# Kernel tuning notes

Measured on AMD Instinct MI355X. Metric: run time of the kernel, lower is better.

Reference implementation:

```python
import jax, jax.numpy as jnp
import numpy as np

N, E = 50000, 800000
IN, HID, OUT, T = 96, 128, 64, 8
THETA = 0.5


def setup_inputs() -> dict:
    key = jax.random.key(0)
    ks = jax.random.split(key, 8)
    x = jax.random.normal(ks[0], (N, IN), dtype=jnp.float32)
    edge_weight = jax.random.uniform(ks[1], (E,), dtype=jnp.float32)
    W1 = jax.random.normal(ks[2], (IN, HID), dtype=jnp.float32) * (2.0 / np.sqrt(IN + HID))
    W2 = jax.random.normal(ks[3], (HID, OUT), dtype=jnp.float32) * (2.0 / np.sqrt(HID + OUT))
    # Bernoulli(1 - theta) masks, fixed per MC sample (created in __init__)
    mask1 = (jax.random.uniform(ks[4], (T, IN, HID)) < (1.0 - THETA)).astype(jnp.float32)
    mask2 = (jax.random.uniform(ks[5], (T, HID, OUT)) < (1.0 - THETA)).astype(jnp.float32)
    src = jax.random.randint(ks[6], (E,), 0, N, dtype=jnp.int32)
    dst = jax.random.randint(ks[7], (E,), 0, N, dtype=jnp.int32)
    return {"x": x, "edge_weight": edge_weight, "W1": W1, "W2": W2,
            "mask1": mask1, "mask2": mask2, "src": src, "dst": dst}


def _spmm(feat, edge_weight, src, dst, n_nodes):
    # u_mul_e('feat','edge_weight') followed by fn.sum onto dst nodes
    msg = feat[src] * edge_weight[:, None]          # [E, D]
    return jax.ops.segment_sum(msg, dst, num_segments=n_nodes)  # [N, D]


def reference(x, edge_weight, W1, W2, mask1, mask2, src, dst):
    n = x.shape[0]
    # first aggregation is mask-independent -> compute once, share across T samples
    agg1 = _spmm(x, edge_weight, src, dst, n)       # [N, IN]

    def per_sample(m1, m2):
        h = jax.nn.relu(agg1 @ (W1 * m1))           # [N, HID]
        agg2 = _spmm(h, edge_weight, src, dst, n)   # [N, HID]
        return agg2 @ (W2 * m2)                     # [N, OUT]

    # stack of the T per-sample outputs (torch version returns a list)
    return jax.vmap(per_sample)(mask1, mask2)       # [T, N, OUT]
```

## Files before the change

### kernel.cpp

```cpp
#include <hip/hip_runtime.h>

#define N_NODES 50000
#define N_EDGES 800000
#define IN_F 96
#define HID_F 128
#define OUT_F 64
#define T_S 8
#define SCAN_B 196

typedef __attribute__((ext_vector_type(8))) short short8;
typedef __attribute__((ext_vector_type(4))) float float4v;

__device__ __forceinline__ float bf2f(unsigned short h) {
    unsigned u = ((unsigned)h) << 16;
    float f;
    __builtin_memcpy(&f, &u, 4);
    return f;
}
__device__ __forceinline__ unsigned short f2bf(float f) {
    unsigned u;
    __builtin_memcpy(&u, &f, 4);
    unsigned r = (u + 0x7fffu + ((u >> 16) & 1u)) >> 16;
    return (unsigned short)r;
}
__device__ __forceinline__ float bf_lo(unsigned u) {
    unsigned v = u << 16;
    float f;
    __builtin_memcpy(&f, &v, 4);
    return f;
}
__device__ __forceinline__ float bf_hi(unsigned u) {
    unsigned v = u & 0xffff0000u;
    float f;
    __builtin_memcpy(&f, &v, 4);
    return f;
}

__global__ void k_count(const int* __restrict__ dst, int* __restrict__ cnt) {
    int e = blockIdx.x * 256 + threadIdx.x;
    if (e < N_EDGES) atomicAdd(&cnt[dst[e]], 1);
}

__global__ __launch_bounds__(256) void k_scan1(const int* __restrict__ cnt,
                                               int* __restrict__ excl,
                                               int* __restrict__ blockSums) {
    __shared__ int buf[256];
    int tid = threadIdx.x;
    int idx = blockIdx.x * 256 + tid;
    int v = (idx < N_NODES) ? cnt[idx] : 0;
    buf[tid] = v;
    __syncthreads();
    for (int off = 1; off < 256; off <<= 1) {
        int t = buf[tid];
        int u = (tid >= off) ? buf[tid - off] : 0;
        __syncthreads();
        buf[tid] = t + u;
        __syncthreads();
    }
    int incl = buf[tid];
    if (idx < N_NODES) excl[idx] = incl - v;
    if (tid == 255) blockSums[blockIdx.x] = incl;
}

__global__ __launch_bounds__(256) void k_scan2(const int* __restrict__ blockSums,
                                               int* __restrict__ blockOff) {
    __shared__ int buf[256];
    int tid = threadIdx.x;
    int v = (tid < SCAN_B) ? blockSums[tid] : 0;
    buf[tid] = v;
    __syncthreads();
    for (int off = 1; off < 256; off <<= 1) {
        int t = buf[tid];
        int u = (tid >= off) ? buf[tid - off] : 0;
        __syncthreads();
        buf[tid] = t + u;
        __syncthreads();
    }
    if (tid < SCAN_B) blockOff[tid] = buf[tid] - v;
}

__global__ __launch_bounds__(256) void k_scan3(const int* __restrict__ excl,
                                               const int* __restrict__ blockOff,
                                               int* __restrict__ row_ptr,
                                               int* __restrict__ cursor) {
    int idx = blockIdx.x * 256 + threadIdx.x;
    if (idx < N_NODES) {
        int p = excl[idx] + blockOff[blockIdx.x];
        row_ptr[idx] = p;
        cursor[idx] = p;
    }
    if (idx == 0) row_ptr[N_NODES] = N_EDGES;
}

__global__ void k_fill(const int* __restrict__ src, const int* __restrict__ dst,
                       const float* __restrict__ ew, int* __restrict__ cursor,
                       int* __restrict__ csr_src, float* __restrict__ csr_w) {
    int e = blockIdx.x * 256 + threadIdx.x;
    if (e < N_EDGES) {
        int d = dst[e];
        int pos = atomicAdd(&cursor[d], 1);
        csr_src[pos] = src[e];
        csr_w[pos] = ew[e];
    }
}

__global__ void k_xb(const float* __restrict__ x, unsigned short* __restrict__ xb) {
    int i = blockIdx.x * 256 + threadIdx.x;
    int idx = i * 4;
    if (idx < N_NODES * IN_F) {
        float4 v = *(const float4*)(x + idx);
        uint2 r;
        r.x = (unsigned)f2bf(v.x) | ((unsigned)f2bf(v.y) << 16);
        r.y = (unsigned)f2bf(v.z) | ((unsigned)f2bf(v.w) << 16);
        *(uint2*)(xb + idx) = r;
    }
}

__global__ __launch_bounds__(256) void k_spmm1(const unsigned short* __restrict__ xb,
                                               const int* __restrict__ row_ptr,
                                               const int* __restrict__ csr_src,
                                               const float* __restrict__ csr_w,
                                               unsigned short* __restrict__ agg1) {
    int wave = threadIdx.x >> 6, lane = threadIdx.x & 63;
    int node = blockIdx.x * 4 + wave;
    if (lane >= 48) return;
    int beg = row_ptr[node], end = row_ptr[node + 1];
    const unsigned* xrow = (const unsigned*)xb;
    float a0 = 0.f, a1 = 0.f;
    int e = beg;
    for (; e + 7 < end; e += 8) {
        int s[8];
        float wv[8];
        unsigned d[8];
#pragma unroll
        for (int i = 0; i < 8; i++) {
            s[i] = csr_src[e + i];
            wv[i] = csr_w[e + i];
        }
#pragma unroll
        for (int i = 0; i < 8; i++) d[i] = xrow[(size_t)s[i] * 48 + lane];
#pragma unroll
        for (int i = 0; i < 8; i++) {
            a0 = fmaf(wv[i], bf_lo(d[i]), a0);
            a1 = fmaf(wv[i], bf_hi(d[i]), a1);
        }
    }
    for (; e < end; e++) {
        int s = csr_src[e];
        float wv = csr_w[e];
        unsigned d = xrow[(size_t)s * 48 + lane];
        a0 = fmaf(wv, bf_lo(d), a0);
        a1 = fmaf(wv, bf_hi(d), a1);
    }
    ((unsigned*)agg1)[(size_t)node * 48 + lane] =
        (unsigned)f2bf(a0) | ((unsigned)f2bf(a1) << 16);
}

__global__ void k_wprep(const float* __restrict__ W1, const float* __restrict__ W2,
                        const float* __restrict__ m1, const float* __restrict__ m2,
                        unsigned short* __restrict__ wf) {
    int gid = blockIdx.x * 256 + threadIdx.x;
    if (gid >= T_S * 20480) return;
    int t = gid / 20480;
    int idx = gid % 20480;
    float val;
    if (idx < 12288) {
        int j = idx & 7, lane = (idx >> 3) & 63, fr = idx >> 9;
        int kk = fr >> 3, nt = fr & 7;
        int k = kk * 32 + (lane >> 4) * 8 + j;
        int n = nt * 16 + (lane & 15);
        val = W1[k * HID_F + n] * m1[((size_t)t * IN_F + k) * HID_F + n];
    } else {
        int i2 = idx - 12288;
        int j = i2 & 7, lane = (i2 >> 3) & 63, fr = i2 >> 9;
        int kk = fr >> 2, ot = fr & 3;
        int k = kk * 32 + (lane >> 4) * 8 + j;
        int o = ot * 16 + (lane & 15);
        val = W2[k * OUT_F + o] * m2[((size_t)t * HID_F + k) * OUT_F + o];
    }
    wf[gid] = f2bf(val);
}

__global__ __launch_bounds__(256) void k_gemm(const unsigned short* __restrict__ agg1,
                                              const unsigned short* __restrict__ wfrags,
                                              unsigned short* __restrict__ P, int tBase,
                                              int nodeStride, int tMul) {
    __shared__ __align__(16) unsigned short ldsW[20480];
    __shared__ __align__(16) unsigned short ldsH[4][2176];
    int t = tBase + blockIdx.y;
    const uint4* wsrc = (const uint4*)(wfrags + (size_t)t * 20480);
    uint4* wdst = (uint4*)ldsW;
    for (int i = threadIdx.x; i < 2560; i += 256) wdst[i] = wsrc[i];
    __syncthreads();

    int wave = threadIdx.x >> 6, lane = threadIdx.x & 63;
    int quad = lane >> 4, l15 = lane & 15;
    int node = blockIdx.x * 64 + wave * 16 + l15;
    bool v = node < N_NODES;

    short8 a[3];
    if (v) {
        const unsigned short* ap = agg1 + (size_t)node * IN_F;
        a[0] = *(const short8*)(ap + 0 * 32 + quad * 8);
        a[1] = *(const short8*)(ap + 1 * 32 + quad * 8);
        a[2] = *(const short8*)(ap + 2 * 32 + quad * 8);
    } else {
        short8 z = {0, 0, 0, 0, 0, 0, 0, 0};
        a[0] = z; a[1] = z; a[2] = z;
    }

    for (int nt = 0; nt < 8; nt++) {
        float4v acc = {0.f, 0.f, 0.f, 0.f};
        for (int kk = 0; kk < 3; kk++) {
            short8 w = *(const short8*)&ldsW[(kk * 8 + nt) * 512 + lane * 8];
            acc = __builtin_amdgcn_mfma_f32_16x16x32_bf16(w, a[kk], acc, 0, 0, 0);
        }
        unsigned h0 = f2bf(fmaxf(acc[0], 0.f));
        unsigned h1 = f2bf(fmaxf(acc[1], 0.f));
        unsigned h2 = f2bf(fmaxf(acc[2], 0.f));
        unsigned h3 = f2bf(fmaxf(acc[3], 0.f));
        uint2 pk;
        pk.x = h0 | (h1 << 16);
        pk.y = h2 | (h3 << 16);
        *(uint2*)&ldsH[wave][l15 * 136 + nt * 16 + quad * 4] = pk;
    }

    short8 hf[4];
    for (int kk = 0; kk < 4; kk++)
        hf[kk] = *(const short8*)&ldsH[wave][l15 * 136 + kk * 32 + quad * 8];

    unsigned short* Pt = P + (size_t)node * nodeStride + (size_t)t * tMul;
    for (int ot = 0; ot < 4; ot++) {
        float4v acc = {0.f, 0.f, 0.f, 0.f};
        for (int kk = 0; kk < 4; kk++) {
            short8 w = *(const short8*)&ldsW[12288 + (kk * 4 + ot) * 512 + lane * 8];
            acc = __builtin_amdgcn_mfma_f32_16x16x32_bf16(w, hf[kk], acc, 0, 0, 0);
        }
        if (v) {
            uint2 pk;
            pk.x = (unsigned)f2bf(acc[0]) | ((unsigned)f2bf(acc[1]) << 16);
            pk.y = (unsigned)f2bf(acc[2]) | ((unsigned)f2bf(acc[3]) << 16);
            *(uint2*)(Pt + ot * 16 + quad * 4) = pk;
        }
    }
}

__global__ __launch_bounds__(256) void k_spmm2(const unsigned short* __restrict__ P,
                                               const int* __restrict__ row_ptr,
                                               const int* __restrict__ csr_src,
                                               const float* __restrict__ csr_w,
                                               float* __restrict__ out) {
    int wave = threadIdx.x >> 6, lane = threadIdx.x & 63;
    int node = blockIdx.x * 4 + wave;
    int beg = row_ptr[node], end = row_ptr[node + 1];
    const uint4* Pl = (const uint4*)P + lane;
    float acc[8] = {0.f, 0.f, 0.f, 0.f, 0.f, 0.f, 0.f, 0.f};
    int e = beg;
    for (; e + 7 < end; e += 8) {
        int s[8];
        float wv[8];
        uint4 d[8];
#pragma unroll
        for (int i = 0; i < 8; i++) {
            s[i] = csr_src[e + i];
            wv[i] = csr_w[e + i];
        }
#pragma unroll
        for (int i = 0; i < 8; i++) d[i] = Pl[(size_t)s[i] * 64];
#pragma unroll
        for (int i = 0; i < 8; i++) {
            acc[0] = fmaf(wv[i], bf_lo(d[i].x), acc[0]);
            acc[1] = fmaf(wv[i], bf_hi(d[i].x), acc[1]);
            acc[2] = fmaf(wv[i], bf_lo(d[i].y), acc[2]);
            acc[3] = fmaf(wv[i], bf_hi(d[i].y), acc[3]);
            acc[4] = fmaf(wv[i], bf_lo(d[i].z), acc[4]);
            acc[5] = fmaf(wv[i], bf_hi(d[i].z), acc[5]);
            acc[6] = fmaf(wv[i], bf_lo(d[i].w), acc[6]);
            acc[7] = fmaf(wv[i], bf_hi(d[i].w), acc[7]);
        }
    }
    for (; e < end; e++) {
        int s = csr_src[e];
        float wv = csr_w[e];
        uint4 d = Pl[(size_t)s * 64];
        acc[0] = fmaf(wv, bf_lo(d.x), acc[0]);
        acc[1] = fmaf(wv, bf_hi(d.x), acc[1]);
        acc[2] = fmaf(wv, bf_lo(d.y), acc[2]);
        acc[3] = fmaf(wv, bf_hi(d.y), acc[3]);
        acc[4] = fmaf(wv, bf_lo(d.z), acc[4]);
        acc[5] = fmaf(wv, bf_hi(d.z), acc[5]);
        acc[6] = fmaf(wv, bf_lo(d.w), acc[6]);
        acc[7] = fmaf(wv, bf_hi(d.w), acc[7]);
    }
    int t = lane >> 3, o = (lane & 7) * 8;
    float* op = out + ((size_t)t * N_NODES + node) * OUT_F + o;
    float4 v0 = {acc[0], acc[1], acc[2], acc[3]};
    float4 v1 = {acc[4], acc[5], acc[6], acc[7]};
    *(float4*)op = v0;
    *(float4*)(op + 4) = v1;
}

__global__ __launch_bounds__(512) void k_spmm2_1t(const unsigned short* __restrict__ P,
                                                  const int* __restrict__ row_ptr,
                                                  const int* __restrict__ csr_src,
                                                  const float* __restrict__ csr_w,
                                                  float* __restrict__ out) {
    int node = blockIdx.x * 8 + (threadIdx.x >> 6);
    int o = threadIdx.x & 63;
    if (node >= N_NODES) return;
    int beg = row_ptr[node], end = row_ptr[node + 1];
    const unsigned short* Pt = P + o;
    float a0 = 0.f, a1 = 0.f, a2 = 0.f, a3 = 0.f;
    int e = beg;
    for (; e + 3 < end; e += 4) {
        int s0 = csr_src[e], s1 = csr_src[e + 1], s2 = csr_src[e + 2], s3 = csr_src[e + 3];
        float w0 = csr_w[e], w1 = csr_w[e + 1], w2 = csr_w[e + 2], w3 = csr_w[e + 3];
        a0 += w0 * bf2f(Pt[(size_t)s0 * OUT_F]);
        a1 += w1 * bf2f(Pt[(size_t)s1 * OUT_F]);
        a2 += w2 * bf2f(Pt[(size_t)s2 * OUT_F]);
        a3 += w3 * bf2f(Pt[(size_t)s3 * OUT_F]);
    }
    for (; e < end; e++) a0 += csr_w[e] * bf2f(Pt[(size_t)csr_src[e] * OUT_F]);
    out[(size_t)node * OUT_F + o] = a0 + a1 + a2 + a3;
}

extern "C" void kernel_launch(void* const* d_in, const int* in_sizes, int n_in,
                              void* d_out, int out_size, void* d_ws, size_t ws_size,
                              hipStream_t stream) {
    const float* x = (const float*)d_in[0];
    const float* ew = (const float*)d_in[1];
    const float* W1 = (const float*)d_in[2];
    const float* W2 = (const float*)d_in[3];
    const float* m1 = (const float*)d_in[4];
    const float* m2 = (const float*)d_in[5];
    const int* src = (const int*)d_in[6];
    const int* dst = (const int*)d_in[7];
    float* out = (float*)d_out;

    char* w = (char*)d_ws;
    size_t off = 0;
    auto alloc = [&](size_t bytes) -> void* {
        void* p = (void*)(w + off);
        off += (bytes + 255) & ~(size_t)255;
        return p;
    };
    int* cnt = (int*)alloc((size_t)N_NODES * 4);
    int* row_ptr = (int*)alloc((size_t)(N_NODES + 1) * 4);
    int* cursor = (int*)alloc((size_t)N_NODES * 4);
    int* excl = (int*)alloc((size_t)N_NODES * 4);
    int* blockSums = (int*)alloc((size_t)SCAN_B * 4);
    int* blockOff = (int*)alloc((size_t)SCAN_B * 4);
    int* csr_src = (int*)alloc((size_t)N_EDGES * 4);
    float* csr_w = (float*)alloc((size_t)N_EDGES * 4);
    unsigned short* agg1 = (unsigned short*)alloc((size_t)N_NODES * IN_F * 2);
    unsigned short* wf = (unsigned short*)alloc((size_t)T_S * 20480 * 2);

    size_t unionBase = off;
    size_t pBytesBatched = (size_t)T_S * N_NODES * OUT_F * 2;
    size_t xbBytes = (size_t)N_NODES * IN_F * 2;
    bool batched = ws_size >= unionBase + (pBytesBatched > xbBytes ? pBytesBatched : xbBytes);
    unsigned short* xb = (unsigned short*)(w + unionBase);
    unsigned short* P = (unsigned short*)(w + unionBase);
    if (!batched) {
        xb = (unsigned short*)(w + unionBase);
        P = (unsigned short*)(w + unionBase + ((xbBytes + 255) & ~(size_t)255));
    }

    hipMemsetAsync(cnt, 0, (size_t)N_NODES * 4, stream);
    k_count<<<N_EDGES / 256, 256, 0, stream>>>(dst, cnt);
    k_scan1<<<SCAN_B, 256, 0, stream>>>(cnt, excl, blockSums);
    k_scan2<<<1, 256, 0, stream>>>(blockSums, blockOff);
    k_scan3<<<SCAN_B, 256, 0, stream>>>(excl, blockOff, row_ptr, cursor);
    k_fill<<<N_EDGES / 256, 256, 0, stream>>>(src, dst, ew, cursor, csr_src, csr_w);
    k_xb<<<(N_NODES * IN_F / 4 + 255) / 256, 256, 0, stream>>>(x, xb);
    k_spmm1<<<N_NODES / 4, 256, 0, stream>>>(xb, row_ptr, csr_src, csr_w, agg1);
    k_wprep<<<(T_S * 20480) / 256, 256, 0, stream>>>(W1, W2, m1, m2, wf);

    if (batched) {
        k_gemm<<<dim3(782, 8), 256, 0, stream>>>(agg1, wf, P, 0, T_S * OUT_F, OUT_F);
        k_spmm2<<<N_NODES / 4, 256, 0, stream>>>(P, row_ptr, csr_src, csr_w, out);
    } else {
        for (int t = 0; t < T_S; t++) {
            k_gemm<<<dim3(782, 1), 256, 0, stream>>>(agg1, wf, P, t, OUT_F, 0);
            k_spmm2_1t<<<6250, 512, 0, stream>>>(P, row_ptr, csr_src, csr_w,
                                                 out + (size_t)t * N_NODES * OUT_F);
        }
    }
}
```

Baseline: 427.7 us.

## Interleave CSR src/weight, add nontemporal hints, amortize GEMM weight load over 4 tiles

Packs csr_src and csr_w into one 8-byte array so each edge needs a single load, and marks the streaming loads and stores nontemporal to keep the gather data resident in cache. The GEMM kernel now handles four 64-node tiles per block, so the 40KB weight copy into LDS happens a quarter as often. A 4-wide remainder loop is added to the SpMM kernels. The trade-off is fewer blocks in the GEMM grid, which lowers parallelism, and nontemporal hints may help or hurt depending on how the cache handles them.

```diff
diff --git a/kernel.cpp b/kernel.cpp
--- a/kernel.cpp
+++ b/kernel.cpp
@@ -10,6 +10,8 @@
 
 typedef __attribute__((ext_vector_type(8))) short short8;
 typedef __attribute__((ext_vector_type(4))) float float4v;
+typedef __attribute__((ext_vector_type(2))) unsigned uint2v;
+typedef __attribute__((ext_vector_type(4))) unsigned uint4v;
 
 __device__ __forceinline__ float bf2f(unsigned short h) {
     unsigned u = ((unsigned)h) << 16;
@@ -94,13 +96,15 @@
 
 __global__ void k_fill(const int* __restrict__ src, const int* __restrict__ dst,
                        const float* __restrict__ ew, int* __restrict__ cursor,
-                       int* __restrict__ csr_src, float* __restrict__ csr_w) {
+                       uint2v* __restrict__ csr) {
     int e = blockIdx.x * 256 + threadIdx.x;
     if (e < N_EDGES) {
         int d = dst[e];
         int pos = atomicAdd(&cursor[d], 1);
-        csr_src[pos] = src[e];
-        csr_w[pos] = ew[e];
+        uint2v c;
+        c.x = (unsigned)src[e];
+        c.y = __float_as_uint(ew[e]);
+        __builtin_nontemporal_store(c, &csr[pos]);
     }
 }
 
@@ -108,18 +112,17 @@
     int i = blockIdx.x * 256 + threadIdx.x;
     int idx = i * 4;
     if (idx < N_NODES * IN_F) {
-        float4 v = *(const float4*)(x + idx);
-        uint2 r;
+        float4v v = __builtin_nontemporal_load((const float4v*)(x + idx));
+        uint2v r;
         r.x = (unsigned)f2bf(v.x) | ((unsigned)f2bf(v.y) << 16);
         r.y = (unsigned)f2bf(v.z) | ((unsigned)f2bf(v.w) << 16);
-        *(uint2*)(xb + idx) = r;
+        *(uint2v*)(xb + idx) = r;
     }
 }
 
 __global__ __launch_bounds__(256) void k_spmm1(const unsigned short* __restrict__ xb,
                                                const int* __restrict__ row_ptr,
-                                               const int* __restrict__ csr_src,
-                                               const float* __restrict__ csr_w,
+                                               const uint2v* __restrict__ csr,
                                                unsigned short* __restrict__ agg1) {
     int wave = threadIdx.x >> 6, lane = threadIdx.x & 63;
     int node = blockIdx.x * 4 + wave;
@@ -129,31 +132,42 @@
     float a0 = 0.f, a1 = 0.f;
     int e = beg;
     for (; e + 7 < end; e += 8) {
-        int s[8];
-        float wv[8];
+        uint2v c[8];
         unsigned d[8];
 #pragma unroll
+        for (int i = 0; i < 8; i++) c[i] = __builtin_nontemporal_load(&csr[e + i]);
+#pragma unroll
+        for (int i = 0; i < 8; i++) d[i] = xrow[(size_t)c[i].x * 48 + lane];
+#pragma unroll
         for (int i = 0; i < 8; i++) {
-            s[i] = csr_src[e + i];
-            wv[i] = csr_w[e + i];
-        }
-#pragma unroll
-        for (int i = 0; i < 8; i++) d[i] = xrow[(size_t)s[i] * 48 + lane];
-#pragma unroll
-        for (int i = 0; i < 8; i++) {
-            a0 = fmaf(wv[i], bf_lo(d[i]), a0);
-            a1 = fmaf(wv[i], bf_hi(d[i]), a1);
+            float wv = __uint_as_float(c[i].y);
+            a0 = fmaf(wv, bf_lo(d[i]), a0);
+            a1 = fmaf(wv, bf_hi(d[i]), a1);
+        }
+    }
+    for (; e + 3 < end; e += 4) {
+        uint2v c[4];
+        unsigned d[4];
+#pragma unroll
+        for (int i = 0; i < 4; i++) c[i] = __builtin_nontemporal_load(&csr[e + i]);
+#pragma unroll
+        for (int i = 0; i < 4; i++) d[i] = xrow[(size_t)c[i].x * 48 + lane];
+#pragma unroll
+        for (int i = 0; i < 4; i++) {
+            float wv = __uint_as_float(c[i].y);
+            a0 = fmaf(wv, bf_lo(d[i]), a0);
+            a1 = fmaf(wv, bf_hi(d[i]), a1);
         }
     }
     for (; e < end; e++) {
-        int s = csr_src[e];
-        float wv = csr_w[e];
-        unsigned d = xrow[(size_t)s * 48 + lane];
+        uint2v c = __builtin_nontemporal_load(&csr[e]);
+        float wv = __uint_as_float(c.y);
+        unsigned d = xrow[(size_t)c.x * 48 + lane];
         a0 = fmaf(wv, bf_lo(d), a0);
         a1 = fmaf(wv, bf_hi(d), a1);
     }
-    ((unsigned*)agg1)[(size_t)node * 48 + lane] =
-        (unsigned)f2bf(a0) | ((unsigned)f2bf(a1) << 16);
+    unsigned pk = (unsigned)f2bf(a0) | ((unsigned)f2bf(a1) << 16);
+    __builtin_nontemporal_store(pk, (unsigned*)agg1 + (size_t)node * 48 + lane);
 }
 
 __global__ void k_wprep(const float* __restrict__ W1, const float* __restrict__ W2,
@@ -195,94 +209,113 @@
 
     int wave = threadIdx.x >> 6, lane = threadIdx.x & 63;
     int quad = lane >> 4, l15 = lane & 15;
-    int node = blockIdx.x * 64 + wave * 16 + l15;
-    bool v = node < N_NODES;
-
-    short8 a[3];
-    if (v) {
-        const unsigned short* ap = agg1 + (size_t)node * IN_F;
-        a[0] = *(const short8*)(ap + 0 * 32 + quad * 8);
-        a[1] = *(const short8*)(ap + 1 * 32 + quad * 8);
-        a[2] = *(const short8*)(ap + 2 * 32 + quad * 8);
-    } else {
-        short8 z = {0, 0, 0, 0, 0, 0, 0, 0};
-        a[0] = z; a[1] = z; a[2] = z;
-    }
-
-    for (int nt = 0; nt < 8; nt++) {
-        float4v acc = {0.f, 0.f, 0.f, 0.f};
-        for (int kk = 0; kk < 3; kk++) {
-            short8 w = *(const short8*)&ldsW[(kk * 8 + nt) * 512 + lane * 8];
-            acc = __builtin_amdgcn_mfma_f32_16x16x32_bf16(w, a[kk], acc, 0, 0, 0);
-        }
-        unsigned h0 = f2bf(fmaxf(acc[0], 0.f));
-        unsigned h1 = f2bf(fmaxf(acc[1], 0.f));
-        unsigned h2 = f2bf(fmaxf(acc[2], 0.f));
-        unsigned h3 = f2bf(fmaxf(acc[3], 0.f));
-        uint2 pk;
-        pk.x = h0 | (h1 << 16);
-        pk.y = h2 | (h3 << 16);
-        *(uint2*)&ldsH[wave][l15 * 136 + nt * 16 + quad * 4] = pk;
-    }
-
-    short8 hf[4];
-    for (int kk = 0; kk < 4; kk++)
-        hf[kk] = *(const short8*)&ldsH[wave][l15 * 136 + kk * 32 + quad * 8];
-
-    unsigned short* Pt = P + (size_t)node * nodeStride + (size_t)t * tMul;
-    for (int ot = 0; ot < 4; ot++) {
-        float4v acc = {0.f, 0.f, 0.f, 0.f};
-        for (int kk = 0; kk < 4; kk++) {
-            short8 w = *(const short8*)&ldsW[12288 + (kk * 4 + ot) * 512 + lane * 8];
-            acc = __builtin_amdgcn_mfma_f32_16x16x32_bf16(w, hf[kk], acc, 0, 0, 0);
-        }
+
+    for (int it = 0; it < 4; it++) {
+        int node = blockIdx.x * 256 + it * 64 + wave * 16 + l15;
+        bool v = node < N_NODES;
+
+        short8 a[3];
         if (v) {
+            const unsigned short* ap = agg1 + (size_t)node * IN_F;
+            a[0] = *(const short8*)(ap + 0 * 32 + quad * 8);
+            a[1] = *(const short8*)(ap + 1 * 32 + quad * 8);
+            a[2] = *(const short8*)(ap + 2 * 32 + quad * 8);
+        } else {
+            short8 z = {0, 0, 0, 0, 0, 0, 0, 0};
+            a[0] = z; a[1] = z; a[2] = z;
+        }
+
+        for (int nt = 0; nt < 8; nt++) {
+            float4v acc = {0.f, 0.f, 0.f, 0.f};
+            for (int kk = 0; kk < 3; kk++) {
+                short8 w = *(const short8*)&ldsW[(kk * 8 + nt) * 512 + lane * 8];
+                acc = __builtin_amdgcn_mfma_f32_16x16x32_bf16(w, a[kk], acc, 0, 0, 0);
+            }
+            unsigned h0 = f2bf(fmaxf(acc[0], 0.f));
+            unsigned h1 = f2bf(fmaxf(acc[1], 0.f));
+            unsigned h2 = f2bf(fmaxf(acc[2], 0.f));
+            unsigned h3 = f2bf(fmaxf(acc[3], 0.f));
             uint2 pk;
-            pk.x = (unsigned)f2bf(acc[0]) | ((unsigned)f2bf(acc[1]) << 16);
-            pk.y = (unsigned)f2bf(acc[2]) | ((unsigned)f2bf(acc[3]) << 16);
-            *(uint2*)(Pt + ot * 16 + quad * 4) = pk;
+            pk.x = h0 | (h1 << 16);
+            pk.y = h2 | (h3 << 16);
+            *(uint2*)&ldsH[wave][l15 * 136 + nt * 16 + quad * 4] = pk;
+        }
+
+        short8 hf[4];
+        for (int kk = 0; kk < 4; kk++)
+            hf[kk] = *(const short8*)&ldsH[wave][l15 * 136 + kk * 32 + quad * 8];
+
+        unsigned short* Pt = P + (size_t)node * nodeStride + (size_t)t * tMul;
+        for (int ot = 0; ot < 4; ot++) {
+            float4v acc = {0.f, 0.f, 0.f, 0.f};
+            for (int kk = 0; kk < 4; kk++) {
+                short8 w = *(const short8*)&ldsW[12288 + (kk * 4 + ot) * 512 + lane * 8];
+                acc = __builtin_amdgcn_mfma_f32_16x16x32_bf16(w, hf[kk], acc, 0, 0, 0);
+            }
+            if (v) {
+                uint2v pk;
+                pk.x = (unsigned)f2bf(acc[0]) | ((unsigned)f2bf(acc[1]) << 16);
+                pk.y = (unsigned)f2bf(acc[2]) | ((unsigned)f2bf(acc[3]) << 16);
+                __builtin_nontemporal_store(pk, (uint2v*)(Pt + ot * 16 + quad * 4));
+            }
         }
     }
 }
 
 __global__ __launch_bounds__(256) void k_spmm2(const unsigned short* __restrict__ P,
                                                const int* __restrict__ row_ptr,
-                                               const int* __restrict__ csr_src,
-                                               const float* __restrict__ csr_w,
+                                               const uint2v* __restrict__ csr,
                                                float* __restrict__ out) {
     int wave = threadIdx.x >> 6, lane = threadIdx.x & 63;
     int node = blockIdx.x * 4 + wave;
     int beg = row_ptr[node], end = row_ptr[node + 1];
-    const uint4* Pl = (const uint4*)P + lane;
+    const uint4v* Pl = (const uint4v*)P + lane;
     float acc[8] = {0.f, 0.f, 0.f, 0.f, 0.f, 0.f, 0.f, 0.f};
     int e = beg;
     for (; e + 7 < end; e += 8) {
-        int s[8];
-        float wv[8];
-        uint4 d[8];
+        uint2v c[8];
+        uint4v d[8];
+#pragma unroll
+        for (int i = 0; i < 8; i++) c[i] = __builtin_nontemporal_load(&csr[e + i]);
+#pragma unroll
+        for (int i = 0; i < 8; i++) d[i] = Pl[(size_t)c[i].x * 64];
 #pragma unroll
         for (int i = 0; i < 8; i++) {
-            s[i] = csr_src[e + i];
-            wv[i] = csr_w[e + i];
-        }
-#pragma unroll
-        for (int i = 0; i < 8; i++) d[i] = Pl[(size_t)s[i] * 64];
-#pragma unroll
-        for (int i = 0; i < 8; i++) {
-            acc[0] = fmaf(wv[i], bf_lo(d[i].x), acc[0]);
-            acc[1] = fmaf(wv[i], bf_hi(d[i].x), acc[1]);
-            acc[2] = fmaf(wv[i], bf_lo(d[i].y), acc[2]);
-            acc[3] = fmaf(wv[i], bf_hi(d[i].y), acc[3]);
-            acc[4] = fmaf(wv[i], bf_lo(d[i].z), acc[4]);
-            acc[5] = fmaf(wv[i], bf_hi(d[i].z), acc[5]);
-            acc[6] = fmaf(wv[i], bf_lo(d[i].w), acc[6]);
-            acc[7] = fmaf(wv[i], bf_hi(d[i].w), acc[7]);
+            float wv = __uint_as_float(c[i].y);
+            acc[0] = fmaf(wv, bf_lo(d[i].x), acc[0]);
+            acc[1] = fmaf(wv, bf_hi(d[i].x), acc[1]);
+            acc[2] = fmaf(wv, bf_lo(d[i].y), acc[2]);
+            acc[3] = fmaf(wv, bf_hi(d[i].y), acc[3]);
+            acc[4] = fmaf(wv, bf_lo(d[i].z), acc[4]);
+            acc[5] = fmaf(wv, bf_hi(d[i].z), acc[5]);
+            acc[6] = fmaf(wv, bf_lo(d[i].w), acc[6]);
+            acc[7] = fmaf(wv, bf_hi(d[i].w), acc[7]);
+        }
+    }
+    for (; e + 3 < end; e += 4) {
+        uint2v c[4];
+        uint4v d[4];
+#pragma unroll
+        for (int i = 0; i < 4; i++) c[i] = __builtin_nontemporal_load(&csr[e + i]);
+#pragma unroll
+        for (int i = 0; i < 4; i++) d[i] = Pl[(size_t)c[i].x * 64];
+#pragma unroll
+        for (int i = 0; i < 4; i++) {
+            float wv = __uint_as_float(c[i].y);
+            acc[0] = fmaf(wv, bf_lo(d[i].x), acc[0]);
+            acc[1] = fmaf(wv, bf_hi(d[i].x), acc[1]);
+            acc[2] = fmaf(wv, bf_lo(d[i].y), acc[2]);
+            acc[3] = fmaf(wv, bf_hi(d[i].y), acc[3]);
+            acc[4] = fmaf(wv, bf_lo(d[i].z), acc[4]);
+            acc[5] = fmaf(wv, bf_hi(d[i].z), acc[5]);
+            acc[6] = fmaf(wv, bf_lo(d[i].w), acc[6]);
+            acc[7] = fmaf(wv, bf_hi(d[i].w), acc[7]);
         }
     }
     for (; e < end; e++) {
-        int s = csr_src[e];
-        float wv = csr_w[e];
-        uint4 d = Pl[(size_t)s * 64];
+        uint2v c = __builtin_nontemporal_load(&csr[e]);
+        float wv = __uint_as_float(c.y);
+        uint4v d = Pl[(size_t)c.x * 64];
         acc[0] = fmaf(wv, bf_lo(d.x), acc[0]);
         acc[1] = fmaf(wv, bf_hi(d.x), acc[1]);
         acc[2] = fmaf(wv, bf_lo(d.y), acc[2]);
@@ -294,16 +327,15 @@
     }
     int t = lane >> 3, o = (lane & 7) * 8;
     float* op = out + ((size_t)t * N_NODES + node) * OUT_F + o;
-    float4 v0 = {acc[0], acc[1], acc[2], acc[3]};
-    float4 v1 = {acc[4], acc[5], acc[6], acc[7]};
-    *(float4*)op = v0;
-    *(float4*)(op + 4) = v1;
+    float4v v0 = {acc[0], acc[1], acc[2], acc[3]};
+    float4v v1 = {acc[4], acc[5], acc[6], acc[7]};
+    __builtin_nontemporal_store(v0, (float4v*)op);
+    __builtin_nontemporal_store(v1, (float4v*)(op + 4));
 }
 
 __global__ __launch_bounds__(512) void k_spmm2_1t(const unsigned short* __restrict__ P,
                                                   const int* __restrict__ row_ptr,
-                                                  const int* __restrict__ csr_src,
-                                                  const float* __restrict__ csr_w,
+                                                  const uint2v* __restrict__ csr,
                                                   float* __restrict__ out) {
     int node = blockIdx.x * 8 + (threadIdx.x >> 6);
     int o = threadIdx.x & 63;
@@ -313,14 +345,19 @@
     float a0 = 0.f, a1 = 0.f, a2 = 0.f, a3 = 0.f;
     int e = beg;
     for (; e + 3 < end; e += 4) {
-        int s0 = csr_src[e], s1 = csr_src[e + 1], s2 = csr_src[e + 2], s3 = csr_src[e + 3];
-        float w0 = csr_w[e], w1 = csr_w[e + 1], w2 = csr_w[e + 2], w3 = csr_w[e + 3];
-        a0 += w0 * bf2f(Pt[(size_t)s0 * OUT_F]);
-        a1 += w1 * bf2f(Pt[(size_t)s1 * OUT_F]);
-        a2 += w2 * bf2f(Pt[(size_t)s2 * OUT_F]);
-        a3 += w3 * bf2f(Pt[(size_t)s3 * OUT_F]);
-    }
-    for (; e < end; e++) a0 += csr_w[e] * bf2f(Pt[(size_t)csr_src[e] * OUT_F]);
+        uint2v c0 = __builtin_nontemporal_load(&csr[e]);
+        uint2v c1 = __builtin_nontemporal_load(&csr[e + 1]);
+        uint2v c2 = __builtin_nontemporal_load(&csr[e + 2]);
+        uint2v c3 = __builtin_nontemporal_load(&csr[e + 3]);
+        a0 += __uint_as_float(c0.y) * bf2f(Pt[(size_t)c0.x * OUT_F]);
+        a1 += __uint_as_float(c1.y) * bf2f(Pt[(size_t)c1.x * OUT_F]);
+        a2 += __uint_as_float(c2.y) * bf2f(Pt[(size_t)c2.x * OUT_F]);
+        a3 += __uint_as_float(c3.y) * bf2f(Pt[(size_t)c3.x * OUT_F]);
+    }
+    for (; e < end; e++) {
+        uint2v c = __builtin_nontemporal_load(&csr[e]);
+        a0 += __uint_as_float(c.y) * bf2f(Pt[(size_t)c.x * OUT_F]);
+    }
     out[(size_t)node * OUT_F + o] = a0 + a1 + a2 + a3;
 }
 
@@ -350,8 +387,7 @@
     int* excl = (int*)alloc((size_t)N_NODES * 4);
     int* blockSums = (int*)alloc((size_t)SCAN_B * 4);
     int* blockOff = (int*)alloc((size_t)SCAN_B * 4);
-    int* csr_src = (int*)alloc((size_t)N_EDGES * 4);
-    float* csr_w = (float*)alloc((size_t)N_EDGES * 4);
+    uint2v* csr = (uint2v*)alloc((size_t)N_EDGES * 8);
     unsigned short* agg1 = (unsigned short*)alloc((size_t)N_NODES * IN_F * 2);
     unsigned short* wf = (unsigned short*)alloc((size_t)T_S * 20480 * 2);
 
@@ -371,18 +407,18 @@
     k_scan1<<<SCAN_B, 256, 0, stream>>>(cnt, excl, blockSums);
     k_scan2<<<1, 256, 0, stream>>>(blockSums, blockOff);
     k_scan3<<<SCAN_B, 256, 0, stream>>>(excl, blockOff, row_ptr, cursor);
-    k_fill<<<N_EDGES / 256, 256, 0, stream>>>(src, dst, ew, cursor, csr_src, csr_w);
+    k_fill<<<N_EDGES / 256, 256, 0, stream>>>(src, dst, ew, cursor, csr);
     k_xb<<<(N_NODES * IN_F / 4 + 255) / 256, 256, 0, stream>>>(x, xb);
-    k_spmm1<<<N_NODES / 4, 256, 0, stream>>>(xb, row_ptr, csr_src, csr_w, agg1);
+    k_spmm1<<<N_NODES / 4, 256, 0, stream>>>(xb, row_ptr, csr, agg1);
     k_wprep<<<(T_S * 20480) / 256, 256, 0, stream>>>(W1, W2, m1, m2, wf);
 
     if (batched) {
-        k_gemm<<<dim3(782, 8), 256, 0, stream>>>(agg1, wf, P, 0, T_S * OUT_F, OUT_F);
-        k_spmm2<<<N_NODES / 4, 256, 0, stream>>>(P, row_ptr, csr_src, csr_w, out);
+        k_gemm<<<dim3(196, 8), 256, 0, stream>>>(agg1, wf, P, 0, T_S * OUT_F, OUT_F);
+        k_spmm2<<<N_NODES / 4, 256, 0, stream>>>(P, row_ptr, csr, out);
     } else {
         for (int t = 0; t < T_S; t++) {
-            k_gemm<<<dim3(782, 1), 256, 0, stream>>>(agg1, wf, P, t, OUT_F, 0);
-            k_spmm2_1t<<<6250, 512, 0, stream>>>(P, row_ptr, csr_src, csr_w,
+            k_gemm<<<dim3(196, 1), 256, 0, stream>>>(agg1, wf, P, t, OUT_F, 0);
+            k_spmm2_1t<<<6250, 512, 0, stream>>>(P, row_ptr, csr,
                                                  out + (size_t)t * N_NODES * OUT_F);
         }
     }
```

After: 423.9 us. Within noise of the previous version (-0.9%).
